# Kernel optimization log

Measured on AMD Instinct MI355X. Metric: run time of the kernel, lower is better.

## Reference

```python
import jax, jax.numpy as jnp
import numpy as np
from jax.ops import segment_sum

N, E, G, D, L = 50000, 800000, 1024, 300, 5
FEAT = 256
EPS = 1e-5


def setup_inputs() -> dict:
    key = jax.random.key(0)
    ks = jax.random.split(key, 20)
    x = jax.random.randint(ks[0], (N, 2), 0, 3)
    edge_index = jax.random.randint(ks[1], (2, E), 0, N)
    edge_attr = jax.random.randint(ks[2], (E, 2), 0, 3)
    batch = jnp.sort(jax.random.randint(ks[3], (N,), 0, G))
    s = 0.05
    x_emb1 = jax.random.normal(ks[4], (119, D), jnp.float32) * s
    x_emb2 = jax.random.normal(ks[5], (3, D), jnp.float32) * s
    W = jax.random.normal(ks[6], (L, D, D), jnp.float32) * (1.0 / np.sqrt(D))
    b = jnp.zeros((L, D), jnp.float32)
    e1 = jax.random.normal(ks[7], (L, 5, 1), jnp.float32) * s
    e2 = jax.random.normal(ks[8], (L, 3, 1), jnp.float32) * s
    gamma = jnp.ones((L, D), jnp.float32)
    beta = jnp.zeros((L, D), jnp.float32)
    feat_w = jax.random.normal(ks[9], (D, FEAT), jnp.float32) * (1.0 / np.sqrt(D))
    feat_b = jnp.zeros((FEAT,), jnp.float32)
    w1 = jax.random.normal(ks[10], (FEAT, FEAT), jnp.float32) * (1.0 / np.sqrt(FEAT))
    b1 = jnp.zeros((FEAT,), jnp.float32)
    w2 = jax.random.normal(ks[11], (FEAT, FEAT // 2), jnp.float32) * (1.0 / np.sqrt(FEAT))
    b2 = jnp.zeros((FEAT // 2,), jnp.float32)
    return dict(x=x, edge_index=edge_index, edge_attr=edge_attr, batch=batch,
                x_emb1=x_emb1, x_emb2=x_emb2, W=W, b=b, e1=e1, e2=e2,
                gamma=gamma, beta=beta, feat_w=feat_w, feat_b=feat_b,
                w1=w1, b1=b1, w2=w2, b2=b2)


def reference(x, edge_index, edge_attr, batch, x_emb1, x_emb2, W, b, e1, e2,
              gamma, beta, feat_w, feat_b, w1, b1, w2, b2):
    row, col = edge_index[0], edge_index[1]
    # node embedding: atom type + chirality
    h = x_emb1[x[:, 0]] + x_emb2[x[:, 1]]  # [N,D]
    for l in range(L):
        hw = h @ W[l]  # [N,D]
        # scalar edge embedding per edge (emb dim is 1 in the source)
        eemb = e1[l, edge_attr[:, 0], 0] + e2[l, edge_attr[:, 1], 0]  # [E]
        msg = hw[row] + eemb[:, None]  # [E,D]
        agg = segment_sum(msg, col, num_segments=N)
        # self loops: edge_attr = (4, 0)
        self_e = e1[l, 4, 0] + e2[l, 0, 0]
        h = agg + hw + self_e + b[l]
        # BatchNorm1d over nodes (batch statistics, biased var)
        mu = jnp.mean(h, axis=0)
        var = jnp.mean((h - mu) ** 2, axis=0)
        h = (h - mu) * jax.lax.rsqrt(var + EPS) * gamma[l] + beta[l]
        if l < L - 1:
            h = jax.nn.relu(h)
    # global mean pool per graph
    sums = segment_sum(h, batch, num_segments=G)  # [G,D]
    cnt = segment_sum(jnp.ones((h.shape[0],), h.dtype), batch, num_segments=G)
    hg = sums / jnp.maximum(cnt, 1.0)[:, None]
    h_feat = hg @ feat_w + feat_b  # [G,FEAT]
    out = jax.nn.relu(h_feat @ w1 + b1) @ w2 + b2  # [G,FEAT//2]
    return (h_feat, out)
```

## Files before the change

kernel.cpp:

```cpp
#include <hip/hip_runtime.h>
#include <hip/hip_bf16.h>

#define NN 50000
#define EE 800000
#define GG 1024
#define DD 300
#define DP 320
#define LL 5
#define FEAT 256

#define AGGB 3136

typedef __bf16 bf16x8 __attribute__((ext_vector_type(8)));
typedef float  f32x4  __attribute__((ext_vector_type(4)));

#define AS1 __attribute__((address_space(1)))
#define AS3 __attribute__((address_space(3)))

__device__ __forceinline__ void dma16(const __hip_bfloat16* g, __hip_bfloat16* l) {
    auto gp = reinterpret_cast<const AS1 char*>(reinterpret_cast<uintptr_t>(g));
    auto lp = reinterpret_cast<AS3 char*>((unsigned int)(uintptr_t)l);
    __builtin_amdgcn_global_load_lds(gp, lp, 16, 0, 0);
}

__device__ __forceinline__ void addbf8(float* a, int4 q) {
    unsigned int u;
    u = (unsigned int)q.x;
    a[0] += __uint_as_float(u << 16); a[1] += __uint_as_float(u & 0xFFFF0000u);
    u = (unsigned int)q.y;
    a[2] += __uint_as_float(u << 16); a[3] += __uint_as_float(u & 0xFFFF0000u);
    u = (unsigned int)q.z;
    a[4] += __uint_as_float(u << 16); a[5] += __uint_as_float(u & 0xFFFF0000u);
    u = (unsigned int)q.w;
    a[6] += __uint_as_float(u << 16); a[7] += __uint_as_float(u & 0xFFFF0000u);
}

__global__ void hist_kernel(const int* __restrict__ ei, int* __restrict__ deg) {
    int e = blockIdx.x * 256 + threadIdx.x;
    atomicAdd(&deg[ei[EE + e]], 1);
}

__global__ void scan1_kernel(const int* __restrict__ deg, int* __restrict__ ptr,
                             int* __restrict__ bsum) {
    __shared__ int buf[256];
    int tid = threadIdx.x;
    int i = blockIdx.x * 256 + tid;
    int v = (i < NN) ? deg[i] : 0;
    buf[tid] = v; __syncthreads();
    for (int off = 1; off < 256; off <<= 1) {
        int t = (tid >= off) ? buf[tid - off] : 0;
        __syncthreads();
        buf[tid] += t;
        __syncthreads();
    }
    if (i < NN) ptr[i + 1] = buf[tid];
    if (tid == 255) bsum[blockIdx.x] = buf[255];
}

__global__ void scan2_kernel(int* __restrict__ bsum) {
    __shared__ int buf[256];
    int tid = threadIdx.x;
    int v = (tid < 196) ? bsum[tid] : 0;
    buf[tid] = v; __syncthreads();
    for (int off = 1; off < 256; off <<= 1) {
        int t = (tid >= off) ? buf[tid - off] : 0;
        __syncthreads();
        buf[tid] += t;
        __syncthreads();
    }
    if (tid < 196) bsum[tid] = buf[tid] - v;
}

__global__ void scan3_kernel(int* __restrict__ ptr, const int* __restrict__ bsum) {
    int i = blockIdx.x * 256 + threadIdx.x;
    if (i < NN) ptr[i + 1] += bsum[blockIdx.x];
    if (i == 0) ptr[0] = 0;
}

__global__ void scatter_kernel(const int* __restrict__ ei, const int* __restrict__ ea,
                               const int* __restrict__ ptr, int* __restrict__ cur,
                               int* __restrict__ srcout) {
    int e = blockIdx.x * 256 + threadIdx.x;
    int r = ei[e], c = ei[EE + e];
    int a0 = ea[e * 2 + 0], a1 = ea[e * 2 + 1];
    int pos = ptr[c] + atomicAdd(&cur[c], 1);
    srcout[pos] = r | (a0 << 16) | (a1 << 18);
}

__global__ void sv_kernel(const int* __restrict__ ptr, const int* __restrict__ src,
                          const float* __restrict__ e1, const float* __restrict__ e2,
                          float* __restrict__ SV) {
    int v = blockIdx.x * 256 + threadIdx.x;
    if (v >= NN) return;
    float c00 = 0.f, c01 = 0.f, c02 = 0.f, c10 = 0.f, c11 = 0.f, c12 = 0.f;
    int beg = ptr[v], end = ptr[v + 1];
    for (int i = beg; i < end; ++i) {
        int p = src[i];
        int e0 = (p >> 16) & 3, ev = (p >> 18) & 3;
        c00 += (e0 == 0); c01 += (e0 == 1); c02 += (e0 == 2);
        c10 += (ev == 0); c11 += (ev == 1); c12 += (ev == 2);
    }
#pragma unroll
    for (int l = 0; l < LL; ++l) {
        float s = c00 * e1[l * 5 + 0] + c01 * e1[l * 5 + 1] + c02 * e1[l * 5 + 2]
                + c10 * e2[l * 3 + 0] + c11 * e2[l * 3 + 1] + c12 * e2[l * 3 + 2];
        SV[l * NN + v] = s;
    }
}

__global__ void repack_kernel(const float* __restrict__ W,
                              __hip_bfloat16* __restrict__ WT) {
    int idx = blockIdx.x * 256 + threadIdx.x;
    int l = idx / (DP * DP);
    int r = idx - l * DP * DP;
    int ntile = r / 51200; r -= ntile * 51200;
    int ktile = r / 10240; r -= ktile * 10240;
    int nn = r >> 6; r &= 63;
    int pu = r >> 3; int e = r & 7;
    int u = pu ^ (nn & 7);
    int n = ntile * 160 + nn;
    int k = ktile * 64 + u * 8 + e;
    float v = 0.f;
    if (n < DD && k < DD) v = W[l * DD * DD + k * DD + n];
    WT[idx] = __float2bfloat16(v);
}

__global__ __launch_bounds__(256) void gemm_kernel(
        const __hip_bfloat16* __restrict__ A, const __hip_bfloat16* __restrict__ BT,
        __hip_bfloat16* __restrict__ C, int M,
        const float* __restrict__ scale, const float* __restrict__ shift,
        const int* __restrict__ x, const float* __restrict__ emb1,
        const float* __restrict__ emb2, int mode) {
    __shared__ __align__(16) char smem[38912];
    __hip_bfloat16* As = reinterpret_cast<__hip_bfloat16*>(smem);
    __hip_bfloat16* Bs = reinterpret_cast<__hip_bfloat16*>(smem + 18432);
    __hip_bfloat16* Cs = reinterpret_cast<__hip_bfloat16*>(smem);
    int tid = threadIdx.x;
    int m0 = blockIdx.x * 128;
    int wave = tid >> 6, lane = tid & 63;
    int wm = (wave >> 1) * 64, wn = (wave & 1) * 80;
    int fm = lane & 15, fu = lane >> 4;

    f32x4 acc[4][5];
#pragma unroll
    for (int i = 0; i < 4; ++i)
#pragma unroll
        for (int j = 0; j < 5; ++j) acc[i][j] = (f32x4){0.f, 0.f, 0.f, 0.f};

    const __hip_bfloat16* btile0 = BT + (size_t)blockIdx.y * 51200;

    for (int k0 = 0; k0 < DP; k0 += 64) {
        __syncthreads();
        const __hip_bfloat16* bt = btile0 + (k0 >> 6) * 10240;
#pragma unroll
        for (int i = 0; i < 5; ++i)
            dma16(bt + (size_t)(tid + i * 256) * 8, Bs + (tid + i * 256) * 8);
#pragma unroll
        for (int u = tid; u < 1024; u += 256) {
            int r = u >> 3, p = u & 7;
            int gr = m0 + r;
            int4 val = make_int4(0, 0, 0, 0);
            if (gr < M) {
                if (mode == 2) {
                    int i0 = x[gr * 2 + 0], i1 = x[gr * 2 + 1];
                    int kb = k0 + p * 8;
                    union { int4 i4; __hip_bfloat16 h[8]; } o;
#pragma unroll
                    for (int j4 = 0; j4 < 2; ++j4) {
                        int kk = kb + j4 * 4;
                        if (kk + 3 < DD) {
                            float4 ea = *reinterpret_cast<const float4*>(emb1 + i0 * DD + kk);
                            float4 eb = *reinterpret_cast<const float4*>(emb2 + i1 * DD + kk);
                            o.h[j4 * 4 + 0] = __float2bfloat16(ea.x + eb.x);
                            o.h[j4 * 4 + 1] = __float2bfloat16(ea.y + eb.y);
                            o.h[j4 * 4 + 2] = __float2bfloat16(ea.z + eb.z);
                            o.h[j4 * 4 + 3] = __float2bfloat16(ea.w + eb.w);
                        } else {
#pragma unroll
                            for (int j = 0; j < 4; ++j) {
                                int k = kk + j;
                                float v = (k < DD) ? emb1[i0 * DD + k] + emb2[i1 * DD + k]
                                                   : 0.f;
                                o.h[j4 * 4 + j] = __float2bfloat16(v);
                            }
                        }
                    }
                    val = o.i4;
                } else {
                    val = *reinterpret_cast<const int4*>(A + (size_t)gr * DP + k0 + p * 8);
                    if (mode == 1) {
                        __hip_bfloat16* hh = reinterpret_cast<__hip_bfloat16*>(&val);
                        int kb = k0 + p * 8;
#pragma unroll
                        for (int j = 0; j < 8; ++j) {
                            float f = fmaf(__bfloat162float(hh[j]), scale[kb + j], shift[kb + j]);
                            hh[j] = __float2bfloat16(fmaxf(f, 0.f));
                        }
                    }
                }
            }
            *reinterpret_cast<int4*>(As + r * 72 + p * 8) = val;
        }
        __syncthreads();
#pragma unroll
        for (int h = 0; h < 2; ++h) {
            bf16x8 af[4], bfr[5];
#pragma unroll
            for (int mt = 0; mt < 4; ++mt)
                af[mt] = *reinterpret_cast<const bf16x8*>(
                    As + (wm + mt * 16 + fm) * 72 + h * 32 + fu * 8);
#pragma unroll
            for (int nt = 0; nt < 5; ++nt) {
                int n = wn + nt * 16 + fm;
                int pu = (h * 4 + fu) ^ (n & 7);
                bfr[nt] = *reinterpret_cast<const bf16x8*>(Bs + n * 64 + pu * 8);
            }
#pragma unroll
            for (int mt = 0; mt < 4; ++mt)
#pragma unroll
                for (int nt = 0; nt < 5; ++nt)
                    acc[mt][nt] = __builtin_amdgcn_mfma_f32_16x16x32_bf16(
                        af[mt], bfr[nt], acc[mt][nt], 0, 0, 0);
        }
    }
    int n0 = blockIdx.y * 160;
    int cc = lane & 15, cr = (lane >> 4) * 4;
#pragma unroll
    for (int h = 0; h < 2; ++h) {
        __syncthreads();
        if ((wave >> 1) == h) {
#pragma unroll
            for (int mt = 0; mt < 4; ++mt)
#pragma unroll
                for (int nt = 0; nt < 5; ++nt)
#pragma unroll
                    for (int r = 0; r < 4; ++r)
                        Cs[(mt * 16 + cr + r) * 168 + wn + nt * 16 + cc] =
                            __float2bfloat16(acc[mt][nt][r]);
        }
        __syncthreads();
#pragma unroll
        for (int u = tid; u < 1280; u += 256) {
            int r = u / 20, c16 = u % 20;
            int row = m0 + h * 64 + r;
            if (row < M)
                *reinterpret_cast<int4*>(C + (size_t)row * DP + n0 + c16 * 8) =
                    *reinterpret_cast<const int4*>(Cs + r * 168 + c16 * 8);
        }
    }
}

__global__ __launch_bounds__(256) void agg_kernel(
        const __hip_bfloat16* __restrict__ HW,
        const int* __restrict__ ptr, const int* __restrict__ src,
        const float* __restrict__ SVl, __hip_bfloat16* __restrict__ AH,
        float* __restrict__ part) {
    int w = threadIdx.x >> 6;
    int lane = threadIdx.x & 63;
    float sx = 0.f, sy = 0.f, sz = 0.f, sw = 0.f, st = 0.f;
    float qx = 0.f, qy = 0.f, qz = 0.f, qw = 0.f, qt = 0.f;

#pragma unroll
    for (int k = 0; k < 4; ++k) {
        int v = blockIdx.x * 16 + w * 4 + k;
        if (v >= NN) break;
        int beg = ptr[v], end = ptr[v + 1];
        const __hip_bfloat16* rv = HW + (size_t)v * DP;
        ushort4 qs = *reinterpret_cast<const ushort4*>(rv + 4 * lane);
        unsigned int ts = reinterpret_cast<const unsigned short*>(rv)[256 + lane];
        float A0x = __uint_as_float((unsigned int)qs.x << 16);
        float A0y = __uint_as_float((unsigned int)qs.y << 16);
        float A0z = __uint_as_float((unsigned int)qs.z << 16);
        float A0w = __uint_as_float((unsigned int)qs.w << 16);
        float A0t = __uint_as_float(ts << 16);
        float A1x = 0.f, A1y = 0.f, A1z = 0.f, A1w = 0.f, A1t = 0.f;
        float A2x = 0.f, A2y = 0.f, A2z = 0.f, A2w = 0.f, A2t = 0.f;
        float A3x = 0.f, A3y = 0.f, A3z = 0.f, A3w = 0.f, A3t = 0.f;
        int i = beg;
        for (; i < end && (i & 3); ++i) {
            int s0 = src[i] & 0xFFFF;
            const __hip_bfloat16* r0 = HW + (size_t)s0 * DP;
            ushort4 q0 = *reinterpret_cast<const ushort4*>(r0 + 4 * lane);
            unsigned int t0 = reinterpret_cast<const unsigned short*>(r0)[256 + lane];
            A0x += __uint_as_float((unsigned int)q0.x << 16);
            A0y += __uint_as_float((unsigned int)q0.y << 16);
            A0z += __uint_as_float((unsigned int)q0.z << 16);
            A0w += __uint_as_float((unsigned int)q0.w << 16);
            A0t += __uint_as_float(t0 << 16);
        }
        for (; i + 4 <= end; i += 4) {
            int4 s4 = *reinterpret_cast<const int4*>(src + i);
            int s0 = s4.x & 0xFFFF, s1 = s4.y & 0xFFFF;
            int s2 = s4.z & 0xFFFF, s3 = s4.w & 0xFFFF;
            const __hip_bfloat16* r0 = HW + (size_t)s0 * DP;
            const __hip_bfloat16* r1 = HW + (size_t)s1 * DP;
            const __hip_bfloat16* r2 = HW + (size_t)s2 * DP;
            const __hip_bfloat16* r3 = HW + (size_t)s3 * DP;
            ushort4 q0 = *reinterpret_cast<const ushort4*>(r0 + 4 * lane);
            ushort4 q1 = *reinterpret_cast<const ushort4*>(r1 + 4 * lane);
            ushort4 q2 = *reinterpret_cast<const ushort4*>(r2 + 4 * lane);
            ushort4 q3 = *reinterpret_cast<const ushort4*>(r3 + 4 * lane);
            unsigned int t0 = reinterpret_cast<const unsigned short*>(r0)[256 + lane];
            unsigned int t1 = reinterpret_cast<const unsigned short*>(r1)[256 + lane];
            unsigned int t2 = reinterpret_cast<const unsigned short*>(r2)[256 + lane];
            unsigned int t3 = reinterpret_cast<const unsigned short*>(r3)[256 + lane];
            A0x += __uint_as_float((unsigned int)q0.x << 16);
            A0y += __uint_as_float((unsigned int)q0.y << 16);
            A0z += __uint_as_float((unsigned int)q0.z << 16);
            A0w += __uint_as_float((unsigned int)q0.w << 16);
            A0t += __uint_as_float(t0 << 16);
            A1x += __uint_as_float((unsigned int)q1.x << 16);
            A1y += __uint_as_float((unsigned int)q1.y << 16);
            A1z += __uint_as_float((unsigned int)q1.z << 16);
            A1w += __uint_as_float((unsigned int)q1.w << 16);
            A1t += __uint_as_float(t1 << 16);
            A2x += __uint_as_float((unsigned int)q2.x << 16);
            A2y += __uint_as_float((unsigned int)q2.y << 16);
            A2z += __uint_as_float((unsigned int)q2.z << 16);
            A2w += __uint_as_float((unsigned int)q2.w << 16);
            A2t += __uint_as_float(t2 << 16);
            A3x += __uint_as_float((unsigned int)q3.x << 16);
            A3y += __uint_as_float((unsigned int)q3.y << 16);
            A3z += __uint_as_float((unsigned int)q3.z << 16);
            A3w += __uint_as_float((unsigned int)q3.w << 16);
            A3t += __uint_as_float(t3 << 16);
        }
        for (; i < end; ++i) {
            int s0 = src[i] & 0xFFFF;
            const __hip_bfloat16* r0 = HW + (size_t)s0 * DP;
            ushort4 q0 = *reinterpret_cast<const ushort4*>(r0 + 4 * lane);
            unsigned int t0 = reinterpret_cast<const unsigned short*>(r0)[256 + lane];
            A0x += __uint_as_float((unsigned int)q0.x << 16);
            A0y += __uint_as_float((unsigned int)q0.y << 16);
            A0z += __uint_as_float((unsigned int)q0.z << 16);
            A0w += __uint_as_float((unsigned int)q0.w << 16);
            A0t += __uint_as_float(t0 << 16);
        }
        float sv = SVl[v];
        float rx = A0x + A1x + A2x + A3x + sv;
        float ry = A0y + A1y + A2y + A3y + sv;
        float rz = A0z + A1z + A2z + A3z + sv;
        float rw = A0w + A1w + A2w + A3w + sv;
        float rt = A0t + A1t + A2t + A3t + sv;
        sx += rx; qx = fmaf(rx, rx, qx);
        sy += ry; qy = fmaf(ry, ry, qy);
        sz += rz; qz = fmaf(rz, rz, qz);
        sw += rw; qw = fmaf(rw, rw, qw);
        st += rt; qt = fmaf(rt, rt, qt);
        __hip_bfloat16* out = AH + (size_t)v * DP;
        union { ushort4 u; __hip_bfloat16 h[4]; } o;
        o.h[0] = __float2bfloat16(rx); o.h[1] = __float2bfloat16(ry);
        o.h[2] = __float2bfloat16(rz); o.h[3] = __float2bfloat16(rw);
        *reinterpret_cast<ushort4*>(out + 4 * lane) = o.u;
        out[256 + lane] = __float2bfloat16(lane < 44 ? rt : 0.f);
    }
    __shared__ float red[4 * 640];
    float* rw_ = red + w * 640;
    rw_[4 * lane + 0] = sx; rw_[4 * lane + 1] = sy;
    rw_[4 * lane + 2] = sz; rw_[4 * lane + 3] = sw;
    rw_[256 + lane] = (lane < 44) ? st : 0.f;
    rw_[320 + 4 * lane + 0] = qx; rw_[320 + 4 * lane + 1] = qy;
    rw_[320 + 4 * lane + 2] = qz; rw_[320 + 4 * lane + 3] = qw;
    rw_[320 + 256 + lane] = (lane < 44) ? qt : 0.f;
    __syncthreads();
    for (int i = threadIdx.x; i < 640; i += 256)
        part[(size_t)blockIdx.x * 640 + i] =
            red[i] + red[640 + i] + red[1280 + i] + red[1920 + i];
}

__global__ void finalize1_kernel(const float* __restrict__ part, float* __restrict__ part2) {
    int b = blockIdx.x;
    const int K = AGGB / 64;
    for (int i = threadIdx.x; i < 640; i += 256) {
        float acc = 0.f;
        for (int k = 0; k < K; ++k)
            acc += part[(size_t)(b * K + k) * 640 + i];
        part2[b * 640 + i] = acc;
    }
}

__global__ void finalize_kernel(const float* __restrict__ part2,
                                const float* __restrict__ gamma_l,
                                const float* __restrict__ beta_l,
                                float* __restrict__ scale, float* __restrict__ shift) {
    int d = threadIdx.x;
    float sc = 0.f, sh = 0.f;
    if (d < DD) {
        float s = 0.f, q = 0.f;
        for (int b = 0; b < 64; ++b) {
            s += part2[b * 640 + d];
            q += part2[b * 640 + 320 + d];
        }
        const float invN = 1.0f / (float)NN;
        float mean = s * invN;
        float var = q * invN - mean * mean;
        var = fmaxf(var, 0.f);
        float rs = rsqrtf(var + 1e-5f);
        sc = rs * gamma_l[d];
        sh = beta_l[d] - mean * sc;
    }
    scale[d] = sc;
    shift[d] = sh;
}

__device__ __forceinline__ int lower_bound_dev(const int* b, int n, int key) {
    int lo = 0, hi = n;
    while (lo < hi) { int mid = (lo + hi) >> 1; if (b[mid] < key) lo = mid + 1; else hi = mid; }
    return lo;
}

__global__ void pool_kernel(const __hip_bfloat16* __restrict__ A, const int* __restrict__ batch,
                            const float* __restrict__ scale, const float* __restrict__ shift,
                            float* __restrict__ HG) {
    int g = blockIdx.x * 4 + (threadIdx.x >> 6);
    int lane = threadIdx.x & 63;
    bool act = lane < 40;
    int lo = lower_bound_dev(batch, NN, g);
    int hi = lower_bound_dev(batch, NN, g + 1);
    const int4 z4 = make_int4(0, 0, 0, 0);
    float a[8];
#pragma unroll
    for (int j = 0; j < 8; ++j) a[j] = 0.f;
    for (int v = lo; v < hi; ++v) {
        int4 q = act ? *reinterpret_cast<const int4*>(A + (size_t)v * DP + 8 * lane) : z4;
        addbf8(a, q);
    }
    if (act) {
        int cnt = hi - lo;
        float inv = 1.0f / (float)(cnt > 0 ? cnt : 1);
        float* out = HG + (size_t)g * DP;
#pragma unroll
        for (int j = 0; j < 8; ++j) {
            int d = 8 * lane + j;
            out[d] = fmaf(a[j] * inv, scale[d], shift[d]);
        }
    }
}

__global__ void feat_kernel(const float* __restrict__ HG,
                            const float* __restrict__ fw,
                            const float* __restrict__ fb,
                            float* __restrict__ HFEAT, float* __restrict__ out0) {
    __shared__ float hgs[DD];
    int g = blockIdx.x, tid = threadIdx.x;
    for (int i = tid; i < DD; i += 256) hgs[i] = HG[(size_t)g * DP + i];
    __syncthreads();
    float acc = fb[tid];
#pragma unroll 4
    for (int k = 0; k < DD; ++k)
        acc = fmaf(hgs[k], fw[k * FEAT + tid], acc);
    HFEAT[g * FEAT + tid] = acc;
    out0[g * FEAT + tid] = acc;
}

__global__ void mlp_kernel(const float* __restrict__ HFEAT,
                           const float* __restrict__ w1, const float* __restrict__ b1,
                           const float* __restrict__ w2, const float* __restrict__ b2,
                           float* __restrict__ out1) {
    __shared__ float hf[FEAT], t[FEAT];
    int g = blockIdx.x, tid = threadIdx.x;
    hf[tid] = HFEAT[g * FEAT + tid];
    __syncthreads();
    float acc = b1[tid];
#pragma unroll 4
    for (int k = 0; k < FEAT; ++k)
        acc = fmaf(hf[k], w1[k * FEAT + tid], acc);
    t[tid] = fmaxf(acc, 0.f);
    __syncthreads();
    if (tid < FEAT / 2) {
        float acc2 = b2[tid];
#pragma unroll 4
        for (int k = 0; k < FEAT; ++k)
            acc2 = fmaf(t[k], w2[k * (FEAT / 2) + tid], acc2);
        out1[g * (FEAT / 2) + tid] = acc2;
    }
}

extern "C" void kernel_launch(void* const* d_in, const int* in_sizes, int n_in,
                              void* d_out, int out_size, void* d_ws, size_t ws_size,
                              hipStream_t stream) {
    const int* x     = (const int*)d_in[0];
    const int* ei    = (const int*)d_in[1];
    const int* ea    = (const int*)d_in[2];
    const int* batch = (const int*)d_in[3];
    const float* emb1  = (const float*)d_in[4];
    const float* emb2  = (const float*)d_in[5];
    const float* W     = (const float*)d_in[6];
    const float* e1    = (const float*)d_in[8];
    const float* e2    = (const float*)d_in[9];
    const float* gamma = (const float*)d_in[10];
    const float* beta  = (const float*)d_in[11];
    const float* fw    = (const float*)d_in[12];
    const float* fb    = (const float*)d_in[13];
    const float* w1    = (const float*)d_in[14];
    const float* b1    = (const float*)d_in[15];
    const float* w2    = (const float*)d_in[16];
    const float* b2    = (const float*)d_in[17];

    char* base = (char*)d_ws;
    size_t off = 0;
    auto carve = [&](size_t bytes) -> void* {
        void* p = base + off;
        off = (off + bytes + 255) & ~(size_t)255;
        return p;
    };
    int*            PTR   = (int*)carve((size_t)(NN + 1) * 4);
    int*            CUR   = (int*)carve((size_t)NN * 4);
    int*            SRC   = (int*)carve((size_t)EE * 4);
    float*          SV    = (float*)carve((size_t)LL * NN * 4);
    int*            BSUM  = (int*)carve(256 * 4);
    float*          PART  = (float*)carve((size_t)AGGB * 640 * 4);
    float*          PART2 = (float*)carve((size_t)64 * 640 * 4);
    float*          SCALE = (float*)carve(DP * 4);
    float*          SHIFT = (float*)carve(DP * 4);
    float*          HG    = (float*)carve((size_t)GG * DP * 4);
    float*          HFEAT = (float*)carve((size_t)GG * FEAT * 4);
    __hip_bfloat16* WT    = (__hip_bfloat16*)carve((size_t)LL * DP * DP * 2);
    __hip_bfloat16* AH    = (__hip_bfloat16*)carve((size_t)NN * DP * 2);
    __hip_bfloat16* HWb   = (__hip_bfloat16*)carve((size_t)NN * DP * 2);

    float* out0 = (float*)d_out;
    float* out1 = (float*)d_out + GG * FEAT;

    hipMemsetAsync(CUR, 0, (size_t)NN * 4, stream);
    hist_kernel<<<EE / 256, 256, 0, stream>>>(ei, CUR);
    scan1_kernel<<<196, 256, 0, stream>>>(CUR, PTR, BSUM);
    scan2_kernel<<<1, 256, 0, stream>>>(BSUM);
    scan3_kernel<<<196, 256, 0, stream>>>(PTR, BSUM);
    hipMemsetAsync(CUR, 0, (size_t)NN * 4, stream);
    scatter_kernel<<<EE / 256, 256, 0, stream>>>(ei, ea, PTR, CUR, SRC);
    sv_kernel<<<196, 256, 0, stream>>>(PTR, SRC, e1, e2, SV);
    repack_kernel<<<(LL * DP * DP) / 256, 256, 0, stream>>>(W, WT);

    for (int l = 0; l < LL; ++l) {
        gemm_kernel<<<dim3(391, 2), 256, 0, stream>>>(
            AH, WT + (size_t)l * DP * DP, HWb, NN, SCALE, SHIFT,
            x, emb1, emb2, l == 0 ? 2 : 1);
        agg_kernel<<<AGGB, 256, 0, stream>>>(HWb, PTR, SRC, SV + (size_t)l * NN, AH, PART);
        finalize1_kernel<<<64, 256, 0, stream>>>(PART, PART2);
        finalize_kernel<<<1, 320, 0, stream>>>(PART2, gamma + l * DD, beta + l * DD, SCALE, SHIFT);
    }

    pool_kernel<<<GG / 4, 256, 0, stream>>>(AH, batch, SCALE, SHIFT, HG);
    feat_kernel<<<GG, 256, 0, stream>>>(HG, fw, fb, HFEAT, out0);
    mlp_kernel<<<GG, 256, 0, stream>>>(HFEAT, w1, b1, w2, b2, out1);
}
```

Measured before the change: 909.2 us.

## Store HW with 304-column stride and gather 16-byte rows in aggregation

```diff
diff --git a/kernel.cpp b/kernel.cpp
--- a/kernel.cpp
+++ b/kernel.cpp
@@ -6,6 +6,7 @@
 #define GG 1024
 #define DD 300
 #define DP 320
+#define HS 304
 #define LL 5
 #define FEAT 256
 
@@ -223,7 +224,7 @@
                         af[mt], bfr[nt], acc[mt][nt], 0, 0, 0);
         }
     }
-    int n0 = blockIdx.y * 160;
+    int base_u = blockIdx.y * 20;
     int cc = lane & 15, cr = (lane >> 4) * 4;
 #pragma unroll
     for (int h = 0; h < 2; ++h) {
@@ -242,9 +243,10 @@
 #pragma unroll
         for (int u = tid; u < 1280; u += 256) {
             int r = u / 20, c16 = u % 20;
+            int gu = base_u + c16;
             int row = m0 + h * 64 + r;
-            if (row < M)
-                *reinterpret_cast<int4*>(C + (size_t)row * DP + n0 + c16 * 8) =
+            if (row < M && gu < 38)
+                *reinterpret_cast<int4*>(C + (size_t)row * HS + gu * 8) =
                     *reinterpret_cast<const int4*>(Cs + r * 168 + c16 * 8);
         }
     }
@@ -257,111 +259,64 @@
         float* __restrict__ part) {
     int w = threadIdx.x >> 6;
     int lane = threadIdx.x & 63;
-    float sx = 0.f, sy = 0.f, sz = 0.f, sw = 0.f, st = 0.f;
-    float qx = 0.f, qy = 0.f, qz = 0.f, qw = 0.f, qt = 0.f;
+    bool act = lane < 38;
+    const int4 z4 = make_int4(0, 0, 0, 0);
+    float bs[8], bq[8];
+#pragma unroll
+    for (int j = 0; j < 8; ++j) { bs[j] = 0.f; bq[j] = 0.f; }
 
 #pragma unroll
     for (int k = 0; k < 4; ++k) {
         int v = blockIdx.x * 16 + w * 4 + k;
         if (v >= NN) break;
         int beg = ptr[v], end = ptr[v + 1];
-        const __hip_bfloat16* rv = HW + (size_t)v * DP;
-        ushort4 qs = *reinterpret_cast<const ushort4*>(rv + 4 * lane);
-        unsigned int ts = reinterpret_cast<const unsigned short*>(rv)[256 + lane];
-        float A0x = __uint_as_float((unsigned int)qs.x << 16);
-        float A0y = __uint_as_float((unsigned int)qs.y << 16);
-        float A0z = __uint_as_float((unsigned int)qs.z << 16);
-        float A0w = __uint_as_float((unsigned int)qs.w << 16);
-        float A0t = __uint_as_float(ts << 16);
-        float A1x = 0.f, A1y = 0.f, A1z = 0.f, A1w = 0.f, A1t = 0.f;
-        float A2x = 0.f, A2y = 0.f, A2z = 0.f, A2w = 0.f, A2t = 0.f;
-        float A3x = 0.f, A3y = 0.f, A3z = 0.f, A3w = 0.f, A3t = 0.f;
+        float a0[8], a1[8], a2[8], a3[8];
+#pragma unroll
+        for (int j = 0; j < 8; ++j) { a0[j] = 0.f; a1[j] = 0.f; a2[j] = 0.f; a3[j] = 0.f; }
+        {
+            int4 q = act ? *reinterpret_cast<const int4*>(HW + (size_t)v * HS + 8 * lane) : z4;
+            addbf8(a0, q);
+        }
         int i = beg;
         for (; i < end && (i & 3); ++i) {
             int s0 = src[i] & 0xFFFF;
-            const __hip_bfloat16* r0 = HW + (size_t)s0 * DP;
-            ushort4 q0 = *reinterpret_cast<const ushort4*>(r0 + 4 * lane);
-            unsigned int t0 = reinterpret_cast<const unsigned short*>(r0)[256 + lane];
-            A0x += __uint_as_float((unsigned int)q0.x << 16);
-            A0y += __uint_as_float((unsigned int)q0.y << 16);
-            A0z += __uint_as_float((unsigned int)q0.z << 16);
-            A0w += __uint_as_float((unsigned int)q0.w << 16);
-            A0t += __uint_as_float(t0 << 16);
+            int4 q = act ? *reinterpret_cast<const int4*>(HW + (size_t)s0 * HS + 8 * lane) : z4;
+            addbf8(a0, q);
         }
         for (; i + 4 <= end; i += 4) {
             int4 s4 = *reinterpret_cast<const int4*>(src + i);
             int s0 = s4.x & 0xFFFF, s1 = s4.y & 0xFFFF;
             int s2 = s4.z & 0xFFFF, s3 = s4.w & 0xFFFF;
-            const __hip_bfloat16* r0 = HW + (size_t)s0 * DP;
-            const __hip_bfloat16* r1 = HW + (size_t)s1 * DP;
-            const __hip_bfloat16* r2 = HW + (size_t)s2 * DP;
-            const __hip_bfloat16* r3 = HW + (size_t)s3 * DP;
-            ushort4 q0 = *reinterpret_cast<const ushort4*>(r0 + 4 * lane);
-            ushort4 q1 = *reinterpret_cast<const ushort4*>(r1 + 4 * lane);
-            ushort4 q2 = *reinterpret_cast<const ushort4*>(r2 + 4 * lane);
-            ushort4 q3 = *reinterpret_cast<const ushort4*>(r3 + 4 * lane);
-            unsigned int t0 = reinterpret_cast<const unsigned short*>(r0)[256 + lane];
-            unsigned int t1 = reinterpret_cast<const unsigned short*>(r1)[256 + lane];
-            unsigned int t2 = reinterpret_cast<const unsigned short*>(r2)[256 + lane];
-            unsigned int t3 = reinterpret_cast<const unsigned short*>(r3)[256 + lane];
-            A0x += __uint_as_float((unsigned int)q0.x << 16);
-            A0y += __uint_as_float((unsigned int)q0.y << 16);
-            A0z += __uint_as_float((unsigned int)q0.z << 16);
-            A0w += __uint_as_float((unsigned int)q0.w << 16);
-            A0t += __uint_as_float(t0 << 16);
-            A1x += __uint_as_float((unsigned int)q1.x << 16);
-            A1y += __uint_as_float((unsigned int)q1.y << 16);
-            A1z += __uint_as_float((unsigned int)q1.z << 16);
-            A1w += __uint_as_float((unsigned int)q1.w << 16);
-            A1t += __uint_as_float(t1 << 16);
-            A2x += __uint_as_float((unsigned int)q2.x << 16);
-            A2y += __uint_as_float((unsigned int)q2.y << 16);
-            A2z += __uint_as_float((unsigned int)q2.z << 16);
-            A2w += __uint_as_float((unsigned int)q2.w << 16);
-            A2t += __uint_as_float(t2 << 16);
-            A3x += __uint_as_float((unsigned int)q3.x << 16);
-            A3y += __uint_as_float((unsigned int)q3.y << 16);
-            A3z += __uint_as_float((unsigned int)q3.z << 16);
-            A3w += __uint_as_float((unsigned int)q3.w << 16);
-            A3t += __uint_as_float(t3 << 16);
+            int4 q0 = act ? *reinterpret_cast<const int4*>(HW + (size_t)s0 * HS + 8 * lane) : z4;
+            int4 q1 = act ? *reinterpret_cast<const int4*>(HW + (size_t)s1 * HS + 8 * lane) : z4;
+            int4 q2 = act ? *reinterpret_cast<const int4*>(HW + (size_t)s2 * HS + 8 * lane) : z4;
+            int4 q3 = act ? *reinterpret_cast<const int4*>(HW + (size_t)s3 * HS + 8 * lane) : z4;
+            addbf8(a0, q0); addbf8(a1, q1); addbf8(a2, q2); addbf8(a3, q3);
         }
         for (; i < end; ++i) {
             int s0 = src[i] & 0xFFFF;
-            const __hip_bfloat16* r0 = HW + (size_t)s0 * DP;
-            ushort4 q0 = *reinterpret_cast<const ushort4*>(r0 + 4 * lane);
-            unsigned int t0 = reinterpret_cast<const unsigned short*>(r0)[256 + lane];
-            A0x += __uint_as_float((unsigned int)q0.x << 16);
-            A0y += __uint_as_float((unsigned int)q0.y << 16);
-            A0z += __uint_as_float((unsigned int)q0.z << 16);
-            A0w += __uint_as_float((unsigned int)q0.w << 16);
-            A0t += __uint_as_float(t0 << 16);
+            int4 q = act ? *reinterpret_cast<const int4*>(HW + (size_t)s0 * HS + 8 * lane) : z4;
+            addbf8(a0, q);
         }
         float sv = SVl[v];
-        float rx = A0x + A1x + A2x + A3x + sv;
-        float ry = A0y + A1y + A2y + A3y + sv;
-        float rz = A0z + A1z + A2z + A3z + sv;
-        float rw = A0w + A1w + A2w + A3w + sv;
-        float rt = A0t + A1t + A2t + A3t + sv;
-        sx += rx; qx = fmaf(rx, rx, qx);
-        sy += ry; qy = fmaf(ry, ry, qy);
-        sz += rz; qz = fmaf(rz, rz, qz);
-        sw += rw; qw = fmaf(rw, rw, qw);
-        st += rt; qt = fmaf(rt, rt, qt);
-        __hip_bfloat16* out = AH + (size_t)v * DP;
-        union { ushort4 u; __hip_bfloat16 h[4]; } o;
-        o.h[0] = __float2bfloat16(rx); o.h[1] = __float2bfloat16(ry);
-        o.h[2] = __float2bfloat16(rz); o.h[3] = __float2bfloat16(rw);
-        *reinterpret_cast<ushort4*>(out + 4 * lane) = o.u;
-        out[256 + lane] = __float2bfloat16(lane < 44 ? rt : 0.f);
+        union { int4 i4; __hip_bfloat16 h[8]; } o;
+#pragma unroll
+        for (int j = 0; j < 8; ++j) {
+            int d = 8 * lane + j;
+            float r = (d < DD) ? (a0[j] + a1[j] + a2[j] + a3[j] + sv) : 0.f;
+            bs[j] += r; bq[j] = fmaf(r, r, bq[j]);
+            o.h[j] = __float2bfloat16(r);
+        }
+        if (lane < 40)
+            *reinterpret_cast<int4*>(AH + (size_t)v * DP + 8 * lane) = o.i4;
     }
     __shared__ float red[4 * 640];
     float* rw_ = red + w * 640;
-    rw_[4 * lane + 0] = sx; rw_[4 * lane + 1] = sy;
-    rw_[4 * lane + 2] = sz; rw_[4 * lane + 3] = sw;
-    rw_[256 + lane] = (lane < 44) ? st : 0.f;
-    rw_[320 + 4 * lane + 0] = qx; rw_[320 + 4 * lane + 1] = qy;
-    rw_[320 + 4 * lane + 2] = qz; rw_[320 + 4 * lane + 3] = qw;
-    rw_[320 + 256 + lane] = (lane < 44) ? qt : 0.f;
+#pragma unroll
+    for (int j = 0; j < 8; ++j) {
+        int d = 8 * lane + j;
+        if (d < 320) { rw_[d] = bs[j]; rw_[320 + d] = bq[j]; }
+    }
     __syncthreads();
     for (int i = threadIdx.x; i < 640; i += 256)
         part[(size_t)blockIdx.x * 640 + i] =
@@ -517,7 +472,7 @@
     float*          HFEAT = (float*)carve((size_t)GG * FEAT * 4);
     __hip_bfloat16* WT    = (__hip_bfloat16*)carve((size_t)LL * DP * DP * 2);
     __hip_bfloat16* AH    = (__hip_bfloat16*)carve((size_t)NN * DP * 2);
-    __hip_bfloat16* HWb   = (__hip_bfloat16*)carve((size_t)NN * DP * 2);
+    __hip_bfloat16* HWb   = (__hip_bfloat16*)carve((size_t)NN * HS * 2);
 
     float* out0 = (float*)d_out;
     float* out1 = (float*)d_out + GG * FEAT;
```

Result: slower. 1.165 ms (+28.2%).
